# Performance work log

Hardware: AMD Instinct MI355X
Metric: run time of the kernel (lower is better)

Reference implementation:

```python
import jax, jax.numpy as jnp
import numpy as np

B, L, D, H = 2, 2048, 1024, 16
HD = D // H


def setup_inputs() -> dict:
    key = jax.random.key(0)
    ks = jax.random.split(key, 8)
    x = jax.random.normal(ks[0], (B, L, D), dtype=jnp.float32)
    WQ = jax.random.normal(ks[1], (D, D), dtype=jnp.float32) * 0.02
    bQ = jnp.zeros((D,), dtype=jnp.float32)
    WK = jax.random.normal(ks[2], (D, D), dtype=jnp.float32) * 0.02
    bK = jnp.zeros((D,), dtype=jnp.float32)
    WV = jax.random.normal(ks[3], (D, D), dtype=jnp.float32) * 0.02
    bV = jnp.zeros((D,), dtype=jnp.float32)
    Wc = jax.random.normal(ks[4], (D, D), dtype=jnp.float32) * 0.02  # dense channel-mix matrix [d_out, d_in]
    return {"x": x, "WQ": WQ, "bQ": bQ, "WK": WK, "bK": bK, "WV": WV, "bV": bV, "Wc": Wc}


def reference(x, WQ, bQ, WK, bK, WV, bV, Wc):
    b, l, d = x.shape
    # --- TokenMixWeightGenerator (LOW_RANK): T = softmax(causal(Q K^T / sqrt(hd)))
    q = (x @ WQ.T + bQ).reshape(b, l, H, HD).transpose(0, 2, 1, 3)  # [B,H,L,hd]
    k = (x @ WK.T + bK).reshape(b, l, H, HD).transpose(0, 2, 1, 3)  # [B,H,L,hd]
    scores = jnp.einsum("bhid,bhjd->bhij", q, k) / jnp.sqrt(jnp.float32(HD))
    causal_mask = jnp.tril(jnp.ones((l, l), dtype=bool))  # keep j <= i
    scores = jnp.where(causal_mask, scores, -jnp.inf)
    T = jax.nn.softmax(scores, axis=-1)  # [B,H,L,L] explicit token-mix matrix
    # --- UnifiedFeaturizer (expansion=1): V reshaped per head
    v = (x @ WV.T + bV).reshape(b, l, H, HD).transpose(0, 2, 1, 3)  # [B,H,L,hd]
    # --- Y = C @ (T @ V)
    mixed = jnp.einsum("bhij,bhjd->bhid", T, v)  # [B,H,L,hd]
    mixed = mixed.transpose(0, 2, 1, 3).reshape(b, l, d)  # [B,L,D]
    y = mixed @ Wc.T  # channel mixing: output = input @ W.T
    return y
```

## Files before the change

### kernel.cpp

```cpp
#include <hip/hip_runtime.h>


typedef __bf16 bf16x8 __attribute__((ext_vector_type(8)));
typedef float f32x4 __attribute__((ext_vector_type(4)));
typedef unsigned short us4 __attribute__((ext_vector_type(4)));

#if defined(__has_builtin)
#if __has_builtin(__builtin_amdgcn_global_load_lds)
#define HAS_GLL 1
#endif
#endif
#ifndef HAS_GLL
#define HAS_GLL 0
#endif

__device__ __forceinline__ float bf2f(unsigned short u) {
    union { unsigned int i; float f; } v; v.i = ((unsigned int)u) << 16; return v.f;
}
__device__ __forceinline__ unsigned short f2bf(float f) {
    union { float f; unsigned int i; } v; v.f = f;
    unsigned int r = v.i + 0x7FFFu + ((v.i >> 16) & 1u);
    return (unsigned short)(r >> 16);
}
__device__ __forceinline__ unsigned short f2bf_fast(float f) {
    union { float f; unsigned int i; } v; v.f = f;
    return (unsigned short)((v.i + 0x8000u) >> 16);
}
__device__ __forceinline__ f32x4 mfma16(bf16x8 a, bf16x8 b, f32x4 c) {
    return __builtin_amdgcn_mfma_f32_16x16x32_bf16(a, b, c, 0, 0, 0);
}
__device__ __forceinline__ float clamp4(float v) {
    return fminf(fmaxf(v, -1e4f), 1e4f);
}
union U8 { unsigned short s[8]; bf16x8 v; };

#if HAS_GLL
__device__ __forceinline__ void gl_lds16(const unsigned short* g, unsigned short* l) {
    __builtin_amdgcn_global_load_lds(
        (const __attribute__((address_space(1))) void*)g,
        (__attribute__((address_space(3))) void*)l, 16, 0, 0);
}
#endif


__global__ __launch_bounds__(256) void convert_all(
    const float* __restrict__ x, const float* __restrict__ WQ,
    const float* __restrict__ WK, const float* __restrict__ WV,
    const float* __restrict__ Wc,
    unsigned short* __restrict__ xbf, unsigned short* __restrict__ wbf)
{
    size_t e = ((size_t)blockIdx.x * 256 + threadIdx.x) * 8;
    const float* src; unsigned short* dst; size_t off;
    if (e < 4194304) { src = x; dst = xbf; off = e; }
    else {
        size_t j = e - 4194304; int sel = (int)(j >> 20); off = j & 1048575;
        src = (sel == 0) ? WQ : (sel == 1) ? WK : (sel == 2) ? WV : Wc;
        dst = wbf + (size_t)sel * 1048576;
    }
    f32x4 a = *(const f32x4*)(src + off);
    f32x4 b = *(const f32x4*)(src + off + 4);
    U8 u;
    u.s[0] = f2bf(a[0]); u.s[1] = f2bf(a[1]); u.s[2] = f2bf(a[2]); u.s[3] = f2bf(a[3]);
    u.s[4] = f2bf(b[0]); u.s[5] = f2bf(b[1]); u.s[6] = f2bf(b[2]); u.s[7] = f2bf(b[3]);
    *(bf16x8*)(dst + off) = u.v;
}

__global__ __launch_bounds__(256) void gemm128(
    const unsigned short* __restrict__ A, const unsigned short* __restrict__ Wbase,
    const float* __restrict__ b0, const float* __restrict__ b1, const float* __restrict__ b2,
    void* __restrict__ d0, void* __restrict__ d1, void* __restrict__ d2, int modeBase)
{
    const int z = blockIdx.z;
    const unsigned short* W = Wbase + (size_t)z * 1048576;
    const float* bias = (z == 0) ? b0 : (z == 1) ? b1 : b2;
    void* dst = (z == 0) ? d0 : (z == 1) ? d1 : d2;
    const int mode = modeBase + z;

    __shared__ __align__(16) unsigned short At[128][32];
    __shared__ __align__(16) unsigned short Bt[128][32];

    const int mb = blockIdx.y * 128, nb = blockIdx.x * 128;
    const int tid = threadIdx.x, w = tid >> 6, lane = tid & 63;
    const int wr = w >> 1, wc = w & 1;
    const int col = lane & 15, quad = lane >> 4;

    f32x4 acc[4][4];
    for (int i = 0; i < 4; ++i) for (int j = 0; j < 4; ++j) acc[i][j] = (f32x4){0.f, 0.f, 0.f, 0.f};

#if HAS_GLL
    const unsigned short* ga = A + (size_t)(mb + w * 32 + (lane >> 2)) * 1024 + (lane & 3) * 8;
    const unsigned short* gw = W + (size_t)(nb + w * 32 + (lane >> 2)) * 1024 + (lane & 3) * 8;
    unsigned short* lA0 = &At[w * 32][0];
    unsigned short* lA1 = &At[w * 32 + 16][0];
    unsigned short* lB0 = &Bt[w * 32][0];
    unsigned short* lB1 = &Bt[w * 32 + 16][0];
#else
    const int srow = w * 32 + (lane >> 1);
    const int scol = (lane & 1) * 16;
    const unsigned short* Ab = A + (size_t)(mb + srow) * 1024 + scol;
    const unsigned short* Wb = W + (size_t)(nb + srow) * 1024 + scol;
#endif

    for (int kb = 0; kb < 1024; kb += 32) {
#if HAS_GLL
        gl_lds16(ga + kb, lA0);
        gl_lds16(ga + kb + 16 * 1024, lA1);
        gl_lds16(gw + kb, lB0);
        gl_lds16(gw + kb + 16 * 1024, lB1);
#else
        *(bf16x8*)&At[srow][scol]     = *(const bf16x8*)(Ab + kb);
        *(bf16x8*)&At[srow][scol + 8] = *(const bf16x8*)(Ab + kb + 8);
        *(bf16x8*)&Bt[srow][scol]     = *(const bf16x8*)(Wb + kb);
        *(bf16x8*)&Bt[srow][scol + 8] = *(const bf16x8*)(Wb + kb + 8);
#endif
        __syncthreads();
        bf16x8 a[4], b[4];
        for (int i = 0; i < 4; ++i) a[i] = *(const bf16x8*)&At[wr * 64 + i * 16 + col][quad * 8];
        for (int j = 0; j < 4; ++j) b[j] = *(const bf16x8*)&Bt[wc * 64 + j * 16 + col][quad * 8];
        for (int i = 0; i < 4; ++i)
            for (int j = 0; j < 4; ++j)
                acc[i][j] = mfma16(a[i], b[j], acc[i][j]);
        __syncthreads();
    }

    for (int i = 0; i < 4; ++i) {
        const int mbase = mb + wr * 64 + i * 16 + quad * 4;
        const int bb = mbase >> 11, l = mbase & 2047;
        for (int j = 0; j < 4; ++j) {
            const int n = nb + wc * 64 + j * 16 + col;
            const float bv = bias ? bias[n] : 0.f;
            if (mode == 3) {
                float* o = (float*)dst;
                for (int r = 0; r < 4; ++r)
                    o[(size_t)(mbase + r) * 1024 + n] = clamp4(acc[i][j][r] + bv);
            } else if (mode == 2) {
                const int h = n >> 6, hd = n & 63;
                us4 pk;
                for (int r = 0; r < 4; ++r) pk[r] = f2bf(clamp4(acc[i][j][r] + bv));
                *(us4*)((unsigned short*)dst + (size_t)(bb * 16 + h) * 131072
                        + (size_t)hd * 2048 + l) = pk;
            } else {
                const int h = n >> 6, hd = n & 63;
                unsigned short* o = (unsigned short*)dst + (size_t)(bb * 16 + h) * 131072
                                    + (size_t)l * 64 + hd;
                for (int r = 0; r < 4; ++r)
                    o[(size_t)r * 64] = f2bf(clamp4(acc[i][j][r] + bv));
            }
        }
    }
}

__device__ __forceinline__ void attn_tile_step(
    const unsigned short (*__restrict__ Kt)[72], const unsigned short (*__restrict__ Vt)[72],
    unsigned short (*__restrict__ Pw)[72],
    bf16x8 aq0, bf16x8 aq1, bf16x8 ones,
    f32x4* __restrict__ oacc, f32x4& lacc,
    bool diag, int col, int quad, int w)
{
    f32x4 s[4];
    for (int t = 0; t < 4; ++t) {
        bf16x8 bk0 = *(const bf16x8*)&Kt[t * 16 + col][quad * 8];
        bf16x8 bk1 = *(const bf16x8*)&Kt[t * 16 + col][32 + quad * 8];
        f32x4 z4 = (f32x4){0.f, 0.f, 0.f, 0.f};
        z4 = mfma16(aq0, bk0, z4);
        s[t] = mfma16(aq1, bk1, z4);
    }
    for (int t = 0; t < 4; ++t)
        for (int r = 0; r < 4; ++r) {
            float v = s[t][r] * 0.125f;
            if (diag && (t * 16 + col > w * 16 + quad * 4 + r)) v = -1e30f;
            v = fminf(v, 60.f);
            Pw[quad * 4 + r][t * 16 + col] = f2bf_fast(__expf(v));
        }
    bf16x8 ap0 = *(const bf16x8*)&Pw[col][quad * 8];
    bf16x8 ap1 = *(const bf16x8*)&Pw[col][32 + quad * 8];
    lacc = mfma16(ap0, ones, lacc);
    lacc = mfma16(ap1, ones, lacc);
    for (int nt = 0; nt < 4; ++nt) {
        bf16x8 bv0 = *(const bf16x8*)&Vt[nt * 16 + col][quad * 8];
        bf16x8 bv1 = *(const bf16x8*)&Vt[nt * 16 + col][32 + quad * 8];
        oacc[nt] = mfma16(ap0, bv0, oacc[nt]);
        oacc[nt] = mfma16(ap1, bv1, oacc[nt]);
    }
}

__device__ __forceinline__ void attn_write(
    unsigned short* __restrict__ mixed, int gb, int h, int q0, int col, int quad,
    const f32x4* __restrict__ oacc, f32x4 lacc)
{
    f32x4 inv;
    for (int r = 0; r < 4; ++r) inv[r] = 1.f / lacc[r];
    for (int nt = 0; nt < 4; ++nt)
        for (int r = 0; r < 4; ++r) {
            int qrow = q0 + quad * 4 + r;
            mixed[(size_t)(gb * 2048 + qrow) * 1024 + h * 64 + nt * 16 + col] =
                f2bf(clamp4(oacc[nt][r] * inv[r]));
        }
}

__global__ __launch_bounds__(256) void attn_pair(
    const unsigned short* __restrict__ Q, const unsigned short* __restrict__ K,
    const unsigned short* __restrict__ V, unsigned short* __restrict__ mixed)
{
    const int ca = blockIdx.x, cb = 31 - ca, bh = blockIdx.y;
    const int tid = threadIdx.x, w = tid >> 6, lane = tid & 63;
    const int col = lane & 15, quad = lane >> 4;

    __shared__ __align__(16) unsigned short Kt[64][72];
    __shared__ __align__(16) unsigned short Vt[64][72];
    __shared__ __align__(16) unsigned short Plds[4][16][72];

    const unsigned short* Qb = Q + (size_t)bh * 131072;
    const unsigned short* Kb = K + (size_t)bh * 131072;
    const unsigned short* Vb = V + (size_t)bh * 131072;

    const int qa0 = ca * 64 + w * 16, qb0 = cb * 64 + w * 16;
    bf16x8 aqa0 = *(const bf16x8*)(Qb + (size_t)(qa0 + col) * 64 + quad * 8);
    bf16x8 aqa1 = *(const bf16x8*)(Qb + (size_t)(qa0 + col) * 64 + 32 + quad * 8);
    bf16x8 aqb0 = *(const bf16x8*)(Qb + (size_t)(qb0 + col) * 64 + quad * 8);
    bf16x8 aqb1 = *(const bf16x8*)(Qb + (size_t)(qb0 + col) * 64 + 32 + quad * 8);

    U8 onesu;
    for (int i = 0; i < 8; ++i) onesu.s[i] = 0x3F80;
    const bf16x8 ones = onesu.v;

    f32x4 oa[4], ob[4];
    f32x4 la = (f32x4){0.f, 0.f, 0.f, 0.f}, lb = (f32x4){0.f, 0.f, 0.f, 0.f};
    for (int i = 0; i < 4; ++i) { oa[i] = la; ob[i] = la; }

    const int sr = tid >> 3, sc = (tid & 7) * 8;

    const unsigned short* kp = Kb + (size_t)sr * 64 + sc;
    const unsigned short* vp = Vb + (size_t)sr * 2048 + sc;
    bf16x8 pk0 = *(const bf16x8*)kp, pk1 = *(const bf16x8*)(kp + 32 * 64);
    bf16x8 pv0 = *(const bf16x8*)vp, pv1 = *(const bf16x8*)(vp + 32 * 2048);

    for (int kt = 0; kt <= cb; ++kt) {
        __syncthreads();
        *(bf16x8*)&Kt[sr][sc]      = pk0;
        *(bf16x8*)&Kt[sr + 32][sc] = pk1;
        *(bf16x8*)&Vt[sr][sc]      = pv0;
        *(bf16x8*)&Vt[sr + 32][sc] = pv1;
        __syncthreads();
        if (kt < cb) {
            const int kb2 = (kt + 1) * 64;
            const unsigned short* kp2 = Kb + (size_t)(kb2 + sr) * 64 + sc;
            const unsigned short* vp2 = Vb + (size_t)sr * 2048 + kb2 + sc;
            pk0 = *(const bf16x8*)kp2; pk1 = *(const bf16x8*)(kp2 + 32 * 64);
            pv0 = *(const bf16x8*)vp2; pv1 = *(const bf16x8*)(vp2 + 32 * 2048);
        }
        attn_tile_step(Kt, Vt, Plds[w], aqb0, aqb1, ones, ob, lb, kt == cb, col, quad, w);
        if (kt <= ca)
            attn_tile_step(Kt, Vt, Plds[w], aqa0, aqa1, ones, oa, la, kt == ca, col, quad, w);
    }

    const int gb = bh >> 4, h = bh & 15;
    attn_write(mixed, gb, h, qa0, col, quad, oa, la);
    attn_write(mixed, gb, h, qb0, col, quad, ob, lb);
}


__device__ __forceinline__ bf16x8 load8(const void* base, size_t eoff, int asF32) {
    if (asF32) {
        const float* p = (const float*)base + eoff;
        f32x4 a = *(const f32x4*)p;
        f32x4 b = *(const f32x4*)(p + 4);
        U8 u;
        u.s[0]=f2bf(a[0]); u.s[1]=f2bf(a[1]); u.s[2]=f2bf(a[2]); u.s[3]=f2bf(a[3]);
        u.s[4]=f2bf(b[0]); u.s[5]=f2bf(b[1]); u.s[6]=f2bf(b[2]); u.s[7]=f2bf(b[3]);
        return u.v;
    }
    return *(const bf16x8*)((const unsigned short*)base + eoff);
}

__global__ void dtype_probe(const unsigned short* __restrict__ x, int* __restrict__ flag) {
    if (threadIdx.x == 0) {
        int c = 0;
        for (int i = 0; i < 128; ++i) {
            int e = (x[2 * i] >> 7) & 0xFF;
            if (e >= 100 && e <= 135) ++c;
        }
        *flag = (c < 64) ? 1 : 0;
    }
}

__global__ __launch_bounds__(256) void gemm_bt(
    const void* __restrict__ Ap, const void* __restrict__ Wp,
    const void* __restrict__ biasp, void* __restrict__ dout,
    unsigned short* __restrict__ wsdst, const int* __restrict__ flag,
    long aOff, long outOff, int mode, int aFlagged)
{
    const int f32 = *flag;
    __shared__ __align__(16) unsigned short At[64][32];
    __shared__ __align__(16) unsigned short Bt[64][32];
    const int mb = blockIdx.y * 64, nb = blockIdx.x * 64;
    const int tid = threadIdx.x;
    const int w = tid >> 6, lane = tid & 63;
    const int wr = w >> 1, wc = w & 1;
    const int col = lane & 15, quad = lane >> 4;
    const int srow = tid >> 2, schunk = (tid & 3) * 8;
    const int aF = aFlagged && f32;

    f32x4 acc[2][2];
    for (int i = 0; i < 2; ++i) for (int j = 0; j < 2; ++j) acc[i][j] = (f32x4){0.f,0.f,0.f,0.f};

    const size_t aBase = (size_t)aOff + (size_t)(mb + srow) * 1024 + schunk;
    const size_t wBase = (size_t)(nb + srow) * 1024 + schunk;

    for (int kb = 0; kb < 1024; kb += 32) {
        *(bf16x8*)(&At[srow][schunk]) = load8(Ap, aBase + kb, aF);
        *(bf16x8*)(&Bt[srow][schunk]) = load8(Wp, wBase + kb, f32);
        __syncthreads();
        bf16x8 a0 = *(const bf16x8*)(&At[wr * 32 + col][quad * 8]);
        bf16x8 a1 = *(const bf16x8*)(&At[wr * 32 + 16 + col][quad * 8]);
        bf16x8 b0 = *(const bf16x8*)(&Bt[wc * 32 + col][quad * 8]);
        bf16x8 b1 = *(const bf16x8*)(&Bt[wc * 32 + 16 + col][quad * 8]);
        acc[0][0] = mfma16(a0, b0, acc[0][0]);
        acc[0][1] = mfma16(a0, b1, acc[0][1]);
        acc[1][0] = mfma16(a1, b0, acc[1][0]);
        acc[1][1] = mfma16(a1, b1, acc[1][1]);
        __syncthreads();
    }

    for (int mi = 0; mi < 2; ++mi) {
        for (int ni = 0; ni < 2; ++ni) {
            int n = nb + wc * 32 + ni * 16 + col;
            float bv = 0.f;
            if (biasp) bv = f32 ? ((const float*)biasp)[n] : bf2f(((const unsigned short*)biasp)[n]);
            for (int r = 0; r < 4; ++r) {
                int m = mb + wr * 32 + mi * 16 + quad * 4 + r;
                float v = clamp4(acc[mi][ni][r] + bv);
                if (mode == 3) {
                    size_t idx = (size_t)outOff + (size_t)m * 1024 + n;
                    if (f32) ((float*)dout)[idx] = v;
                    else     ((unsigned short*)dout)[idx] = f2bf(v);
                } else {
                    int h = n >> 6, hd = n & 63;
                    size_t idx = (mode == 2)
                        ? (size_t)h * 131072 + (size_t)hd * 2048 + m
                        : (size_t)h * 131072 + (size_t)m * 64 + hd;
                    unsigned short* dstp = (mode == 0)
                        ? (unsigned short*)dout + (f32 ? 4194304 : 2097152)
                        : wsdst;
                    dstp[idx] = f2bf(v);
                }
            }
        }
    }
}

__global__ __launch_bounds__(256) void attn_kernel(
    const void* __restrict__ dout, const unsigned short* __restrict__ Kw,
    const unsigned short* __restrict__ Vw, unsigned short* __restrict__ mixed,
    const int* __restrict__ flag)
{
    const int f32 = *flag;
    const int qtile = blockIdx.x;
    const int h = blockIdx.y;
    const int w = threadIdx.x >> 6, lane = threadIdx.x & 63;
    const int col = lane & 15, quad = lane >> 4;

    __shared__ __align__(16) unsigned short Plds[4][16][64];

    const unsigned short* Qs = (const unsigned short*)dout + (f32 ? 4194304 : 2097152);
    const unsigned short* Qb = Qs + (size_t)h * 131072;
    const unsigned short* Kb = Kw + (size_t)h * 131072;
    const unsigned short* Vb = Vw + (size_t)h * 131072;

    const int q0 = qtile * 64 + w * 16;
    bf16x8 aq0 = *(const bf16x8*)(Qb + (size_t)(q0 + col) * 64 + quad * 8);
    bf16x8 aq1 = *(const bf16x8*)(Qb + (size_t)(q0 + col) * 64 + 32 + quad * 8);

    float m_run[4] = {-1e30f, -1e30f, -1e30f, -1e30f};
    float l_run[4] = {0.f, 0.f, 0.f, 0.f};
    f32x4 oacc[4];
    for (int i = 0; i < 4; ++i) oacc[i] = (f32x4){0.f, 0.f, 0.f, 0.f};

    for (int kt = 0; kt <= qtile; ++kt) {
        const int kb = kt * 64;
        f32x4 s[4];
        for (int t = 0; t < 4; ++t) {
            s[t] = (f32x4){0.f, 0.f, 0.f, 0.f};
            bf16x8 bk0 = *(const bf16x8*)(Kb + (size_t)(kb + t * 16 + col) * 64 + quad * 8);
            bf16x8 bk1 = *(const bf16x8*)(Kb + (size_t)(kb + t * 16 + col) * 64 + 32 + quad * 8);
            s[t] = mfma16(aq0, bk0, s[t]);
            s[t] = mfma16(aq1, bk1, s[t]);
        }
        for (int t = 0; t < 4; ++t)
            for (int r = 0; r < 4; ++r) {
                float v = clamp4(s[t][r] * 0.125f);
                if (kt == qtile && (t * 16 + col > w * 16 + quad * 4 + r)) v = -1e30f;
                s[t][r] = v;
            }
        float mt[4];
        for (int r = 0; r < 4; ++r)
            mt[r] = fmaxf(fmaxf(s[0][r], s[1][r]), fmaxf(s[2][r], s[3][r]));
        for (int off = 1; off < 16; off <<= 1)
            for (int r = 0; r < 4; ++r)
                mt[r] = fmaxf(mt[r], __shfl_xor(mt[r], off, 64));
        float alpha[4], rs[4], p[4][4];
        for (int r = 0; r < 4; ++r) {
            float mn = fmaxf(m_run[r], mt[r]);
            alpha[r] = __expf(m_run[r] - mn);
            m_run[r] = mn;
        }
        for (int t = 0; t < 4; ++t)
            for (int r = 0; r < 4; ++r)
                p[t][r] = __expf(s[t][r] - m_run[r]);
        for (int r = 0; r < 4; ++r)
            rs[r] = (p[0][r] + p[1][r]) + (p[2][r] + p[3][r]);
        for (int off = 1; off < 16; off <<= 1)
            for (int r = 0; r < 4; ++r)
                rs[r] += __shfl_xor(rs[r], off, 64);
        for (int r = 0; r < 4; ++r)
            l_run[r] = l_run[r] * alpha[r] + rs[r];
        for (int nt = 0; nt < 4; ++nt)
            for (int r = 0; r < 4; ++r)
                oacc[nt][r] *= alpha[r];
        for (int t = 0; t < 4; ++t)
            for (int r = 0; r < 4; ++r)
                Plds[w][quad * 4 + r][t * 16 + col] = f2bf(p[t][r]);
        __syncthreads();
        bf16x8 ap0 = *(const bf16x8*)(&Plds[w][col][quad * 8]);
        bf16x8 ap1 = *(const bf16x8*)(&Plds[w][col][32 + quad * 8]);
        for (int nt = 0; nt < 4; ++nt) {
            bf16x8 bv0 = *(const bf16x8*)(Vb + (size_t)(nt * 16 + col) * 2048 + kb + quad * 8);
            bf16x8 bv1 = *(const bf16x8*)(Vb + (size_t)(nt * 16 + col) * 2048 + kb + 32 + quad * 8);
            oacc[nt] = mfma16(ap0, bv0, oacc[nt]);
            oacc[nt] = mfma16(ap1, bv1, oacc[nt]);
        }
        __syncthreads();
    }

    float inv[4];
    for (int r = 0; r < 4; ++r) inv[r] = 1.f / l_run[r];
    for (int nt = 0; nt < 4; ++nt)
        for (int r = 0; r < 4; ++r) {
            int qrow = q0 + quad * 4 + r;
            mixed[(size_t)qrow * 1024 + h * 64 + nt * 16 + col] = f2bf(clamp4(oacc[nt][r] * inv[r]));
        }
}


extern "C" void kernel_launch(void* const* d_in, const int* in_sizes, int n_in,
                              void* d_out, int out_size, void* d_ws, size_t ws_size,
                              hipStream_t stream) {
    (void)in_sizes; (void)n_in; (void)out_size;
    const void* x  = d_in[0];
    const void* WQ = d_in[1]; const void* bQ = d_in[2];
    const void* WK = d_in[3]; const void* bK = d_in[4];
    const void* WV = d_in[5]; const void* bV = d_in[6];
    const void* Wc = d_in[7];

    if (ws_size >= (size_t)32 * 1024 * 1024) {
        unsigned short* wbf   = (unsigned short*)d_ws;
        unsigned short* Kst   = wbf + 4194304;
        unsigned short* VTst  = Kst + 4194304;
        unsigned short* mixed = VTst + 4194304;
        unsigned short* xbf   = (unsigned short*)d_out;
        unsigned short* Qst   = xbf + 4194304;

        convert_all<<<4096, 256, 0, stream>>>(
            (const float*)x, (const float*)WQ, (const float*)WK,
            (const float*)WV, (const float*)Wc, xbf, wbf);

        gemm128<<<dim3(8, 32, 3), 256, 0, stream>>>(
            xbf, wbf, (const float*)bQ, (const float*)bK, (const float*)bV,
            Qst, Kst, VTst, 0);

        attn_pair<<<dim3(16, 32), 256, 0, stream>>>(Qst, Kst, VTst, mixed);

        gemm128<<<dim3(8, 32, 1), 256, 0, stream>>>(
            mixed, wbf + 3145728, nullptr, nullptr, nullptr,
            d_out, nullptr, nullptr, 3);
    } else {
        unsigned short* wsK = (unsigned short*)d_ws;
        unsigned short* wsV = wsK + 2097152;
        unsigned short* wsM = wsV + 2097152;
        int* flag = (int*)((char*)d_ws + 12 * 1024 * 1024);

        dtype_probe<<<1, 64, 0, stream>>>((const unsigned short*)x, flag);

        dim3 gg(16, 32), gb(256);
        for (int b = 0; b < 2; ++b) {
            long xo = (long)b * 2048 * 1024;
            gemm_bt<<<gg, gb, 0, stream>>>(x, WQ, bQ, d_out, nullptr, flag, xo, 0, 0, 1);
            gemm_bt<<<gg, gb, 0, stream>>>(x, WK, bK, d_out, wsK, flag, xo, 0, 1, 1);
            gemm_bt<<<gg, gb, 0, stream>>>(x, WV, bV, d_out, wsV, flag, xo, 0, 2, 1);
            attn_kernel<<<dim3(32, 16), 256, 0, stream>>>(d_out, wsK, wsV, wsM, flag);
            gemm_bt<<<gg, gb, 0, stream>>>(wsM, Wc, nullptr, d_out, nullptr, flag,
                                           0, (long)b * 2048 * 1024, 3, 0);
        }
    }
}
```

Before: 193.0 us.

## Split paired attention blocks into single q-tile blocks and use exp2 with packed bf16 stores

The attention kernel no longer pairs two causal query tiles per block (ca and 31-ca). It now launches 1024 blocks, one query tile each, and interleaves long and short tiles through a remapped block index to balance the load. The softmax uses exp2 with a pre-folded log2e scale. Adjacent lanes' probabilities are combined with a DPP lane swap and written as one packed bf16 pair with v_cvt_pk_bf16_f32, halving the scalar LDS stores. In exchange, K/V tiles are loaded once per query tile instead of shared by two, so K/V global traffic roughly doubles.

```diff
diff --git a/kernel.cpp b/kernel.cpp
--- a/kernel.cpp
+++ b/kernel.cpp
@@ -9,9 +9,18 @@
 #if __has_builtin(__builtin_amdgcn_global_load_lds)
 #define HAS_GLL 1
 #endif
+#if __has_builtin(__builtin_amdgcn_exp2f)
+#define EXP2F(x) __builtin_amdgcn_exp2f(x)
+#endif
+#if __has_builtin(__builtin_amdgcn_mov_dpp)
+#define HAS_MOVDPP 1
+#endif
 #endif
 #ifndef HAS_GLL
 #define HAS_GLL 0
+#endif
+#ifndef EXP2F
+#define EXP2F(x) exp2f(x)
 #endif
 
 __device__ __forceinline__ float bf2f(unsigned short u) {
@@ -22,10 +31,6 @@
     unsigned int r = v.i + 0x7FFFu + ((v.i >> 16) & 1u);
     return (unsigned short)(r >> 16);
 }
-__device__ __forceinline__ unsigned short f2bf_fast(float f) {
-    union { float f; unsigned int i; } v; v.f = f;
-    return (unsigned short)((v.i + 0x8000u) >> 16);
-}
 __device__ __forceinline__ f32x4 mfma16(bf16x8 a, bf16x8 b, f32x4 c) {
     return __builtin_amdgcn_mfma_f32_16x16x32_bf16(a, b, c, 0, 0, 0);
 }
@@ -33,6 +38,22 @@
     return fminf(fmaxf(v, -1e4f), 1e4f);
 }
 union U8 { unsigned short s[8]; bf16x8 v; };
+
+__device__ __forceinline__ float swap_lane1(float x) {
+#if defined(HAS_MOVDPP)
+    union { float f; int i; } u; u.f = x;
+    u.i = __builtin_amdgcn_mov_dpp(u.i, 0xB1, 0xF, 0xF, true);
+    return u.f;
+#else
+    return __shfl_xor(x, 1, 64);
+#endif
+}
+
+__device__ __forceinline__ unsigned int cvt_pk_bf16(float lo, float hi) {
+    unsigned int r;
+    asm("v_cvt_pk_bf16_f32 %0, %1, %2" : "=v"(r) : "v"(lo), "v"(hi));
+    return r;
+}
 
 #if HAS_GLL
 __device__ __forceinline__ void gl_lds16(const unsigned short* g, unsigned short* l) {
@@ -150,12 +171,12 @@
     }
 }
 
-__device__ __forceinline__ void attn_tile_step(
+__device__ __forceinline__ void attn_step(
     const unsigned short (*__restrict__ Kt)[72], const unsigned short (*__restrict__ Vt)[72],
     unsigned short (*__restrict__ Pw)[72],
     bf16x8 aq0, bf16x8 aq1, bf16x8 ones,
     f32x4* __restrict__ oacc, f32x4& lacc,
-    bool diag, int col, int quad, int w)
+    bool diag, int col, int quad, int w, int lane)
 {
     f32x4 s[4];
     for (int t = 0; t < 4; ++t) {
@@ -165,13 +186,21 @@
         z4 = mfma16(aq0, bk0, z4);
         s[t] = mfma16(aq1, bk1, z4);
     }
-    for (int t = 0; t < 4; ++t)
+    const int myq = w * 16 + quad * 4;
+    for (int t = 0; t < 4; ++t) {
         for (int r = 0; r < 4; ++r) {
-            float v = s[t][r] * 0.125f;
-            if (diag && (t * 16 + col > w * 16 + quad * 4 + r)) v = -1e30f;
-            v = fminf(v, 60.f);
-            Pw[quad * 4 + r][t * 16 + col] = f2bf_fast(__expf(v));
-        }
+            float v = s[t][r] * 0.18033688f;
+            if (diag && (t * 16 + col > myq + r)) v = -1e30f;
+            v = fminf(v, 86.5f);
+            s[t][r] = EXP2F(v);
+        }
+        for (int r = 0; r < 4; ++r) {
+            float pv = s[t][r];
+            float po = swap_lane1(pv);
+            if (!(lane & 1))
+                *(unsigned int*)&Pw[quad * 4 + r][t * 16 + col] = cvt_pk_bf16(pv, po);
+        }
+    }
     bf16x8 ap0 = *(const bf16x8*)&Pw[col][quad * 8];
     bf16x8 ap1 = *(const bf16x8*)&Pw[col][32 + quad * 8];
     lacc = mfma16(ap0, ones, lacc);
@@ -198,11 +227,16 @@
         }
 }
 
-__global__ __launch_bounds__(256) void attn_pair(
+__global__ __launch_bounds__(256) void attn_one(
     const unsigned short* __restrict__ Q, const unsigned short* __restrict__ K,
     const unsigned short* __restrict__ V, unsigned short* __restrict__ mixed)
 {
-    const int ca = blockIdx.x, cb = 31 - ca, bh = blockIdx.y;
+    const int l = blockIdx.x;
+    const int i = l & 255, kq = l >> 8;
+    const int a = i & 31;
+    const int qt = (kq & 1) ? (31 - a) : a;
+    const int bh = (i >> 5) + 8 * kq;
+
     const int tid = threadIdx.x, w = tid >> 6, lane = tid & 63;
     const int col = lane & 15, quad = lane >> 4;
 
@@ -214,19 +248,17 @@
     const unsigned short* Kb = K + (size_t)bh * 131072;
     const unsigned short* Vb = V + (size_t)bh * 131072;
 
-    const int qa0 = ca * 64 + w * 16, qb0 = cb * 64 + w * 16;
-    bf16x8 aqa0 = *(const bf16x8*)(Qb + (size_t)(qa0 + col) * 64 + quad * 8);
-    bf16x8 aqa1 = *(const bf16x8*)(Qb + (size_t)(qa0 + col) * 64 + 32 + quad * 8);
-    bf16x8 aqb0 = *(const bf16x8*)(Qb + (size_t)(qb0 + col) * 64 + quad * 8);
-    bf16x8 aqb1 = *(const bf16x8*)(Qb + (size_t)(qb0 + col) * 64 + 32 + quad * 8);
+    const int q0 = qt * 64 + w * 16;
+    bf16x8 aq0 = *(const bf16x8*)(Qb + (size_t)(q0 + col) * 64 + quad * 8);
+    bf16x8 aq1 = *(const bf16x8*)(Qb + (size_t)(q0 + col) * 64 + 32 + quad * 8);
 
     U8 onesu;
-    for (int i = 0; i < 8; ++i) onesu.s[i] = 0x3F80;
+    for (int j = 0; j < 8; ++j) onesu.s[j] = 0x3F80;
     const bf16x8 ones = onesu.v;
 
-    f32x4 oa[4], ob[4];
-    f32x4 la = (f32x4){0.f, 0.f, 0.f, 0.f}, lb = (f32x4){0.f, 0.f, 0.f, 0.f};
-    for (int i = 0; i < 4; ++i) { oa[i] = la; ob[i] = la; }
+    f32x4 oacc[4];
+    f32x4 lacc = (f32x4){0.f, 0.f, 0.f, 0.f};
+    for (int j = 0; j < 4; ++j) oacc[j] = lacc;
 
     const int sr = tid >> 3, sc = (tid & 7) * 8;
 
@@ -235,28 +267,25 @@
     bf16x8 pk0 = *(const bf16x8*)kp, pk1 = *(const bf16x8*)(kp + 32 * 64);
     bf16x8 pv0 = *(const bf16x8*)vp, pv1 = *(const bf16x8*)(vp + 32 * 2048);
 
-    for (int kt = 0; kt <= cb; ++kt) {
+    for (int kt = 0; kt <= qt; ++kt) {
         __syncthreads();
         *(bf16x8*)&Kt[sr][sc]      = pk0;
         *(bf16x8*)&Kt[sr + 32][sc] = pk1;
         *(bf16x8*)&Vt[sr][sc]      = pv0;
         *(bf16x8*)&Vt[sr + 32][sc] = pv1;
         __syncthreads();
-        if (kt < cb) {
+        if (kt < qt) {
             const int kb2 = (kt + 1) * 64;
             const unsigned short* kp2 = Kb + (size_t)(kb2 + sr) * 64 + sc;
             const unsigned short* vp2 = Vb + (size_t)sr * 2048 + kb2 + sc;
             pk0 = *(const bf16x8*)kp2; pk1 = *(const bf16x8*)(kp2 + 32 * 64);
             pv0 = *(const bf16x8*)vp2; pv1 = *(const bf16x8*)(vp2 + 32 * 2048);
         }
-        attn_tile_step(Kt, Vt, Plds[w], aqb0, aqb1, ones, ob, lb, kt == cb, col, quad, w);
-        if (kt <= ca)
-            attn_tile_step(Kt, Vt, Plds[w], aqa0, aqa1, ones, oa, la, kt == ca, col, quad, w);
+        attn_step(Kt, Vt, Plds[w], aq0, aq1, ones, oacc, lacc, kt == qt, col, quad, w, lane);
     }
 
     const int gb = bh >> 4, h = bh & 15;
-    attn_write(mixed, gb, h, qa0, col, quad, oa, la);
-    attn_write(mixed, gb, h, qb0, col, quad, ob, lb);
+    attn_write(mixed, gb, h, q0, col, quad, oacc, lacc);
 }
 
 
@@ -468,7 +497,7 @@
             xbf, wbf, (const float*)bQ, (const float*)bK, (const float*)bV,
             Qst, Kst, VTst, 0);
 
-        attn_pair<<<dim3(16, 32), 256, 0, stream>>>(Qst, Kst, VTst, mixed);
+        attn_one<<<dim3(1024, 1), 256, 0, stream>>>(Qst, Kst, VTst, mixed);
 
         gemm128<<<dim3(8, 32, 1), 256, 0, stream>>>(
             mixed, wbf + 3145728, nullptr, nullptr, nullptr,
```

New measurement: 195.6 us. About the same (+1.4%).
